# Kernel optimization log

Hardware: AMD Instinct MI355X
Metric: run time of the kernel (lower is better)

The kernel has to match this reference:

```python
import jax, jax.numpy as jnp
import numpy as np

ALPHA = 0.2  # LeakyReLU negative slope
EPS = 1e-6


def gam(x):
    # relu6(x+3)/3 + eps
    return jnp.clip(x + 3.0, 0.0, 6.0) / 3.0 + EPS


def leaky(x):
    return jnp.where(x >= 0, x, ALPHA * x)


def relu_bt(x):
    # threshold at detached inf-norm of input: min(leaky_relu(x), ||x||_inf)
    t = jax.lax.stop_gradient(jnp.max(jnp.abs(x)))
    return jnp.minimum(leaky(x), t)


def setup_inputs() -> dict:
    key = jax.random.key(0)
    ks = jax.random.split(key, 8)
    N, E, Din, Dout = 100000, 1600000, 256, 64
    return {
        "input": jax.random.normal(ks[0], (N, Din), dtype=jnp.float32),
        "edge": jax.random.randint(ks[1], (2, E), 0, N, dtype=jnp.int32),
        "W_high": jax.random.normal(ks[2], (Din, Dout), dtype=jnp.float32) * 0.06,
        "W_low": jax.random.normal(ks[3], (Din, Dout), dtype=jnp.float32) * 0.06,
        "a_high": jax.random.normal(ks[4], (1, 4 * Dout), dtype=jnp.float32) * 0.09,
        "a_low": jax.random.normal(ks[5], (1, 4 * Dout), dtype=jnp.float32) * 0.09,
        "c_high": jax.random.uniform(ks[6], (1, 1), dtype=jnp.float32),
        "c_low": jax.random.uniform(ks[7], (1, 1), dtype=jnp.float32),
    }


def reference(input, edge, W_high, W_low, a_high, a_low, c_high, c_low):
    N = input.shape[0]
    F = W_high.shape[1]
    src, dst = edge[0], edge[1]

    theta_high = gam(c_high) / 2.0  # [1,1]
    theta_low = gam(c_low) / 2.0

    h_high = relu_bt(input @ W_high)  # [N,F]
    h_low = relu_bt(input @ W_low)

    hh_s, hh_d = h_high[src], h_high[dst]  # [E,F]
    hl_s, hl_d = h_low[src], h_low[dst]

    ah = a_high[0]
    al = a_low[0]
    # a . [h_i, h_j, h_i+h_j, h_i-h_j] folded into per-endpoint coefficients
    # NOTE: original code uses h_high for the first two blocks of the LOW branch too.
    score_high = hh_s @ (ah[:F] + ah[2 * F:3 * F] + ah[3 * F:]) \
               + hh_d @ (ah[F:2 * F] + ah[2 * F:3 * F] - ah[3 * F:])  # [E]
    score_low = hh_s @ al[:F] + hh_d @ al[F:2 * F] \
              + hl_s @ (al[2 * F:3 * F] + al[3 * F:]) \
              + hl_d @ (al[2 * F:3 * F] - al[3 * F:])

    e_high = jnp.exp(-leaky(score_high / jnp.linalg.norm(a_high)))  # [E]
    e_low = jnp.exp(-leaky(score_low / jnp.linalg.norm(a_low)))

    # sparse COO spmm: rowsum and weighted aggregation
    rowsum_high = jax.ops.segment_sum(e_high, src, num_segments=N)[:, None]  # [N,1]
    rowsum_low = jax.ops.segment_sum(e_low, src, num_segments=N)[:, None]
    hp_high = jax.ops.segment_sum(e_high[:, None] * hh_d, src, num_segments=N)  # [N,F]
    hp_low = jax.ops.segment_sum(e_low[:, None] * hl_d, src, num_segments=N)

    hp_high = hp_high / (rowsum_high + theta_high)
    hp_low = hp_low / (rowsum_low + theta_low)

    # concat=True branch
    return relu_bt(jnp.concatenate([hp_high, hp_low], axis=1))  # [N,2F]
```

## Files before the change

kernel.cpp:

```cpp
#include <hip/hip_runtime.h>
#include <hip/hip_bf16.h>
#include <hip/hip_fp16.h>
#include <math.h>

typedef unsigned short ushort_t;
typedef unsigned int uint_t;
typedef __attribute__((ext_vector_type(8))) short short8;
typedef __attribute__((ext_vector_type(4))) float floatx4;
typedef __attribute__((ext_vector_type(4))) uint_t uintx4;

#define ALPHA 0.2f
#define CAP 64
#define NXCD 8

__device__ __forceinline__ float leaky(float x) { return x >= 0.0f ? x : ALPHA * x; }

__device__ __forceinline__ float bf2f(ushort_t u) {
    union { uint_t i; float f; } v; v.i = ((uint_t)u) << 16; return v.f;
}
__device__ __forceinline__ float bflo(uint_t p) {
    union { uint_t i; float f; } v; v.i = p << 16; return v.f;
}
__device__ __forceinline__ float bfhi(uint_t p) {
    union { uint_t i; float f; } v; v.i = p & 0xffff0000u; return v.f;
}
__device__ __forceinline__ ushort_t f2bf(float f) {
    union { float f; uint_t i; } v; v.f = f;
    return (ushort_t)((v.i + 0x8000u) >> 16);
}
__device__ __forceinline__ uint_t pack_bf2(float a, float b) {
    union { float f; uint_t i; } ua, ub; ua.f = a; ub.f = b;
    return ((ua.i + 0x8000u) >> 16) | ((ub.i + 0x8000u) & 0xffff0000u);
}

__global__ void prep_wtrans_kernel(const float* __restrict__ Wh, const float* __restrict__ Wl,
                                   ushort_t* __restrict__ WTg,
                                   const float* __restrict__ ah, const float* __restrict__ al,
                                   const float* __restrict__ ch, const float* __restrict__ cl,
                                   float* __restrict__ coef, float* __restrict__ consts) {
    int t = threadIdx.x;
    if (blockIdx.x < 128) {
        int c = blockIdx.x;
        float v = (c < 64) ? Wh[t * 64 + c] : Wl[t * 64 + (c - 64)];
        WTg[c * 256 + t] = f2bf(v);
        return;
    }
    __shared__ float red[256];
    float va = ah[t];
    red[t] = va * va;
    __syncthreads();
    for (int s = 128; s > 0; s >>= 1) { if (t < s) red[t] += red[t + s]; __syncthreads(); }
    float sum_h = red[0];
    __syncthreads();
    float vb = al[t];
    red[t] = vb * vb;
    __syncthreads();
    for (int s = 128; s > 0; s >>= 1) { if (t < s) red[t] += red[t + s]; __syncthreads(); }
    float sum_l = red[0];

    if (t == 0) {
        consts[0] = 1.0f / sqrtf(sum_h);
        consts[1] = 1.0f / sqrtf(sum_l);
        float c = ch[0];
        float g = fminf(fmaxf(c + 3.0f, 0.0f), 6.0f) / 3.0f + 1e-6f;
        consts[2] = g * 0.5f;
        c = cl[0];
        g = fminf(fmaxf(c + 3.0f, 0.0f), 6.0f) / 3.0f + 1e-6f;
        consts[3] = g * 0.5f;
    }
    if (t < 128) {
        int f = t;
        float c0, c1, c2, c3;
        if (f < 64) {
            c0 = ah[f] + ah[128 + f] + ah[192 + f];
            c1 = ah[64 + f] + ah[128 + f] - ah[192 + f];
            c2 = al[f];
            c3 = al[64 + f];
        } else {
            int g = f - 64;
            c0 = 0.0f;
            c1 = 0.0f;
            c2 = al[128 + g] + al[192 + g];
            c3 = al[128 + g] - al[192 + g];
        }
        coef[0 * 128 + f] = c0;
        coef[1 * 128 + f] = c1;
        coef[2 * 128 + f] = c2;
        coef[3 * 128 + f] = c3;
    }
}

__global__ __launch_bounds__(256, 4) void gemm_kernel(const float* __restrict__ in,
                                                      const ushort_t* __restrict__ WTg,
                                                      const float* __restrict__ coef,
                                                      ushort_t* __restrict__ hcat,
                                                      float* __restrict__ s4, int N) {
    __shared__ ushort_t WT[128 * 128];
    __shared__ float coefS[512];
    int tid = threadIdx.x;
    for (int i = tid; i < 512; i += 256) coefS[i] = coef[i];

    int wave = tid >> 6, lane = tid & 63;
    int quad = lane >> 4, m16 = lane & 15;
    int rowbase = blockIdx.x * 64 + wave * 16;
    int arow = rowbase + m16;
    if (arow >= N) arow = N - 1;

    floatx4 acc[8];
#pragma unroll
    for (int ct = 0; ct < 8; ++ct) acc[ct] = (floatx4){0.0f, 0.0f, 0.0f, 0.0f};

    const uint4* WTg4 = (const uint4*)WTg;

#pragma unroll
    for (int kh = 0; kh < 2; ++kh) {
        if (kh) __syncthreads();
        for (int i = tid; i < 2048; i += 256) {
            int c = i >> 4, j = i & 15;
            int sj = j ^ (c & 7);
            uint4 v = WTg4[c * 32 + kh * 16 + j];
            *(uint4*)&WT[c * 128 + sj * 8] = v;
        }
        __syncthreads();
#pragma unroll
        for (int ks = 0; ks < 4; ++ks) {
            const float* ap = in + (size_t)arow * 256 + kh * 128 + ks * 32 + quad * 8;
            float4 a0 = *(const float4*)ap;
            float4 a1 = *(const float4*)(ap + 4);
            union { uintx4 u; short8 s; } av;
            av.u[0] = pack_bf2(a0.x, a0.y);
            av.u[1] = pack_bf2(a0.z, a0.w);
            av.u[2] = pack_bf2(a1.x, a1.y);
            av.u[3] = pack_bf2(a1.z, a1.w);
#pragma unroll
            for (int ct = 0; ct < 8; ++ct) {
                int c = ct * 16 + m16;
                int sch = (ks * 4 + quad) ^ (c & 7);
                short8 b = *(const short8*)&WT[c * 128 + sch * 8];
                acc[ct] = __builtin_amdgcn_mfma_f32_16x16x32_bf16(av.s, b, acc[ct], 0, 0, 0);
            }
        }
    }

    float hv[8][4];
#pragma unroll
    for (int ct = 0; ct < 8; ++ct) {
#pragma unroll
        for (int r = 0; r < 4; ++r) {
            int row = rowbase + quad * 4 + r;
            float v = leaky(acc[ct][r]);
            hv[ct][r] = v;
            if (row < N) hcat[(size_t)row * 128 + ct * 16 + m16] = f2bf(v);
        }
    }
#pragma unroll
    for (int r = 0; r < 4; ++r) {
        int row = rowbase + quad * 4 + r;
        float p0 = 0, p1 = 0, p2 = 0, p3 = 0;
#pragma unroll
        for (int ct = 0; ct < 8; ++ct) {
            int c = ct * 16 + m16;
            float h = hv[ct][r];
            p0 += coefS[c] * h;
            p1 += coefS[128 + c] * h;
            p2 += coefS[256 + c] * h;
            p3 += coefS[384 + c] * h;
        }
#pragma unroll
        for (int off = 1; off < 16; off <<= 1) {
            p0 += __shfl_xor(p0, off);
            p1 += __shfl_xor(p1, off);
            p2 += __shfl_xor(p2, off);
            p3 += __shfl_xor(p3, off);
        }
        if (m16 == 0 && row < N) {
            floatx4 v = {p0, p1, p2, p3};
            *(floatx4*)&s4[(size_t)row * 4] = v;
        }
    }
}

__global__ __launch_bounds__(256) void scatter_kernel(const int* __restrict__ edge,
                                                      int* __restrict__ cursor,
                                                      uint_t* __restrict__ elist,
                                                      int E, int N) {
    int xcd = blockIdx.x & (NXCD - 1);
    int chunk = blockIdx.x >> 3;
    int nchunks = gridDim.x >> 3;
    int TN = (N + NXCD - 1) / NXCD;
    int lo = xcd * TN;
    int hiN = lo + TN;
    int stride = nchunks * 256;
    for (int e = chunk * 256 + threadIdx.x; e < E; e += stride) {
        int src = edge[e];
        if (src >= lo && src < hiN) {
            int dst = edge[E + e];
            int pos = atomicAdd(&cursor[src], 1);
            if (pos < CAP) elist[(size_t)src * CAP + pos] = (uint_t)dst;
        }
    }
}

__global__ __launch_bounds__(256) void aggregate_kernel(const int* __restrict__ deg,
                                                        const uint_t* __restrict__ elist,
                                                        const ushort_t* __restrict__ hcat,
                                                        const float* __restrict__ s4,
                                                        const float* __restrict__ consts,
                                                        float* __restrict__ out, int N) {
    int w = (blockIdx.x * blockDim.x + threadIdx.x) >> 6;
    int lane = threadIdx.x & 63;
    if (w >= N) return;
    int d = deg[w];
    if (d > CAP) d = CAP;

    float s_own_h = s4[(size_t)w * 4 + 0];
    float s_own_l = s4[(size_t)w * 4 + 2];
    float inv_h = consts[0], inv_l = consts[1];
    int dst = 0;
    float wh = 0.0f, wl = 0.0f;
    if (lane < d) {
        dst = (int)elist[(size_t)w * CAP + lane];
        float4 sv = *(const float4*)&s4[(size_t)dst * 4];
        wh = __expf(-leaky((s_own_h + sv.y) * inv_h));
        wl = __expf(-leaky((s_own_l + sv.w) * inv_l));
    }
    uint_t wp = (uint_t)__half_as_ushort(__float2half(wh))
              | ((uint_t)__half_as_ushort(__float2half(wl)) << 16);
    float rsh = wh, rsl = wl;
#pragma unroll
    for (int off = 1; off < 64; off <<= 1) {
        rsh += __shfl_xor(rsh, off);
        rsl += __shfl_xor(rsl, off);
    }

    bool hi = lane < 32;
    int wsh = hi ? 0 : 16;
    const ushort_t* hbase = hcat + lane * 2;

    float a0 = 0, a1 = 0, b0 = 0, b1 = 0;
    int j = 0;
    for (; j + 4 <= d; j += 4) {
        int d0 = __shfl(dst, j);
        int d1 = __shfl(dst, j + 1);
        int d2 = __shfl(dst, j + 2);
        int d3 = __shfl(dst, j + 3);
        uint_t u0 = (uint_t)__shfl((int)wp, j);
        uint_t u1 = (uint_t)__shfl((int)wp, j + 1);
        uint_t u2 = (uint_t)__shfl((int)wp, j + 2);
        uint_t u3 = (uint_t)__shfl((int)wp, j + 3);
        uint_t p0 = *(const uint_t*)&hbase[(size_t)d0 * 128];
        uint_t p1 = *(const uint_t*)&hbase[(size_t)d1 * 128];
        uint_t p2 = *(const uint_t*)&hbase[(size_t)d2 * 128];
        uint_t p3 = *(const uint_t*)&hbase[(size_t)d3 * 128];
        float w0 = __half2float(__ushort_as_half((ushort_t)(u0 >> wsh)));
        float w1 = __half2float(__ushort_as_half((ushort_t)(u1 >> wsh)));
        float w2 = __half2float(__ushort_as_half((ushort_t)(u2 >> wsh)));
        float w3 = __half2float(__ushort_as_half((ushort_t)(u3 >> wsh)));
        a0 += w0 * bflo(p0); a1 += w0 * bfhi(p0);
        b0 += w1 * bflo(p1); b1 += w1 * bfhi(p1);
        a0 += w2 * bflo(p2); a1 += w2 * bfhi(p2);
        b0 += w3 * bflo(p3); b1 += w3 * bfhi(p3);
    }
    for (; j < d; ++j) {
        int dj = __shfl(dst, j);
        uint_t uj = (uint_t)__shfl((int)wp, j);
        uint_t p = *(const uint_t*)&hbase[(size_t)dj * 128];
        float wt = __half2float(__ushort_as_half((ushort_t)(uj >> wsh)));
        a0 += wt * bflo(p);
        a1 += wt * bfhi(p);
    }

    float acc0 = a0 + b0;
    float acc1 = a1 + b1;
    float rsum = hi ? rsh : rsl;
    float theta = hi ? consts[2] : consts[3];
    float inv = 1.0f / (rsum + theta);
    float2 r;
    r.x = leaky(acc0 * inv);
    r.y = leaky(acc1 * inv);
    *(float2*)&out[(size_t)w * 128 + lane * 2] = r;
}

extern "C" void kernel_launch(void* const* d_in, const int* in_sizes, int n_in,
                              void* d_out, int out_size, void* d_ws, size_t ws_size,
                              hipStream_t stream) {
    const float* input = (const float*)d_in[0];
    const int* edge = (const int*)d_in[1];
    const float* Wh = (const float*)d_in[2];
    const float* Wl = (const float*)d_in[3];
    const float* ah = (const float*)d_in[4];
    const float* al = (const float*)d_in[5];
    const float* ch = (const float*)d_in[6];
    const float* cl = (const float*)d_in[7];
    int N = in_sizes[0] / 256;
    int E = in_sizes[1] / 2;
    float* out = (float*)d_out;

    char* ws = (char*)d_ws;
    size_t off = 0;
    uint_t* elist = (uint_t*)(ws + off);     off += (size_t)N * CAP * 4;
    ushort_t* hcat = (ushort_t*)(ws + off);  off += (size_t)N * 128 * 2;
    float* s4 = (float*)(ws + off);          off += (size_t)N * 4 * 4;
    int* cursor = (int*)(ws + off);          off += (size_t)N * 4;
    ushort_t* WTg = (ushort_t*)(ws + off);   off += 128 * 256 * 2;
    float* coef = (float*)(ws + off);        off += 4 * 128 * 4;
    float* consts = (float*)(ws + off);      off += 64;

    hipMemsetAsync(cursor, 0, (size_t)N * 4, stream);
    prep_wtrans_kernel<<<129, 256, 0, stream>>>(Wh, Wl, WTg, ah, al, ch, cl, coef, consts);
    gemm_kernel<<<(N + 63) / 64, 256, 0, stream>>>(input, WTg, coef, hcat, s4, N);
    int nchunks = (E + 256 * 8 - 1) / (256 * 8);
    scatter_kernel<<<nchunks * NXCD, 256, 0, stream>>>(edge, cursor, elist, E, N);
    aggregate_kernel<<<(N + 3) / 4, 256, 0, stream>>>(cursor, elist, hcat, s4, consts, out, N);
}
```

Measured before the change: 356.5 us.

## Merge edge scatter into GEMM launch so both run concurrently

Fuses the edge-bucketing scatter and the projection GEMM into one launch. The first Gscat blocks do the scatter and the remaining blocks do the GEMM, so the latency-bound atomic scatter overlaps with the compute-bound GEMM and one kernel launch boundary goes away. The scatter now reads four source indices per thread with nontemporal vector loads and uses a fixed chunk count. The GEMM input loads also become nontemporal. The combined kernel carries the GEMM's shared memory footprint into the scatter blocks, which can lower their occupancy.

```diff
diff --git a/kernel.cpp b/kernel.cpp
--- a/kernel.cpp
+++ b/kernel.cpp
@@ -8,6 +8,7 @@
 typedef __attribute__((ext_vector_type(8))) short short8;
 typedef __attribute__((ext_vector_type(4))) float floatx4;
 typedef __attribute__((ext_vector_type(4))) uint_t uintx4;
+typedef __attribute__((ext_vector_type(4))) int intx4;
 
 #define ALPHA 0.2f
 #define CAP 64
@@ -90,19 +91,51 @@
     }
 }
 
-__global__ __launch_bounds__(256, 4) void gemm_kernel(const float* __restrict__ in,
-                                                      const ushort_t* __restrict__ WTg,
-                                                      const float* __restrict__ coef,
-                                                      ushort_t* __restrict__ hcat,
-                                                      float* __restrict__ s4, int N) {
+__global__ __launch_bounds__(256, 4) void gemm_scatter_kernel(
+        const float* __restrict__ in, const ushort_t* __restrict__ WTg,
+        const float* __restrict__ coef, ushort_t* __restrict__ hcat,
+        float* __restrict__ s4, const int* __restrict__ edge,
+        int* __restrict__ cursor, uint_t* __restrict__ elist,
+        int N, int E, int Gscat) {
     __shared__ ushort_t WT[128 * 128];
     __shared__ float coefS[512];
+
+    if ((int)blockIdx.x < Gscat) {
+        int xcd = blockIdx.x & (NXCD - 1);
+        int chunk = blockIdx.x >> 3;
+        int nchunks = Gscat >> 3;
+        int TN = (N + NXCD - 1) / NXCD;
+        int lo = xcd * TN;
+        int hiN = lo + TN;
+        int base = (chunk * 256 + threadIdx.x) * 4;
+        int stride = nchunks * 256 * 4;
+        for (int e = base; e < E; e += stride) {
+            intx4 sv;
+            if (e + 4 <= E) {
+                sv = __builtin_nontemporal_load((const intx4*)(edge + e));
+            } else {
+#pragma unroll
+                for (int j = 0; j < 4; ++j) sv[j] = (e + j < E) ? edge[e + j] : -1;
+            }
+#pragma unroll
+            for (int j = 0; j < 4; ++j) {
+                int src = sv[j];
+                if (src >= lo && src < hiN) {
+                    int dst = __builtin_nontemporal_load(edge + E + e + j);
+                    int pos = atomicAdd(&cursor[src], 1);
+                    if (pos < CAP) elist[(size_t)src * CAP + pos] = (uint_t)dst;
+                }
+            }
+        }
+        return;
+    }
+
     int tid = threadIdx.x;
     for (int i = tid; i < 512; i += 256) coefS[i] = coef[i];
 
     int wave = tid >> 6, lane = tid & 63;
     int quad = lane >> 4, m16 = lane & 15;
-    int rowbase = blockIdx.x * 64 + wave * 16;
+    int rowbase = (blockIdx.x - Gscat) * 64 + wave * 16;
     int arow = rowbase + m16;
     if (arow >= N) arow = N - 1;
 
@@ -124,14 +157,14 @@
         __syncthreads();
 #pragma unroll
         for (int ks = 0; ks < 4; ++ks) {
-            const float* ap = in + (size_t)arow * 256 + kh * 128 + ks * 32 + quad * 8;
-            float4 a0 = *(const float4*)ap;
-            float4 a1 = *(const float4*)(ap + 4);
+            const floatx4* ap = (const floatx4*)(in + (size_t)arow * 256 + kh * 128 + ks * 32 + quad * 8);
+            floatx4 a0 = __builtin_nontemporal_load(ap);
+            floatx4 a1 = __builtin_nontemporal_load(ap + 1);
             union { uintx4 u; short8 s; } av;
-            av.u[0] = pack_bf2(a0.x, a0.y);
-            av.u[1] = pack_bf2(a0.z, a0.w);
-            av.u[2] = pack_bf2(a1.x, a1.y);
-            av.u[3] = pack_bf2(a1.z, a1.w);
+            av.u[0] = pack_bf2(a0[0], a0[1]);
+            av.u[1] = pack_bf2(a0[2], a0[3]);
+            av.u[2] = pack_bf2(a1[0], a1[1]);
+            av.u[3] = pack_bf2(a1[2], a1[3]);
 #pragma unroll
             for (int ct = 0; ct < 8; ++ct) {
                 int c = ct * 16 + m16;
@@ -176,27 +209,6 @@
         if (m16 == 0 && row < N) {
             floatx4 v = {p0, p1, p2, p3};
             *(floatx4*)&s4[(size_t)row * 4] = v;
-        }
-    }
-}
-
-__global__ __launch_bounds__(256) void scatter_kernel(const int* __restrict__ edge,
-                                                      int* __restrict__ cursor,
-                                                      uint_t* __restrict__ elist,
-                                                      int E, int N) {
-    int xcd = blockIdx.x & (NXCD - 1);
-    int chunk = blockIdx.x >> 3;
-    int nchunks = gridDim.x >> 3;
-    int TN = (N + NXCD - 1) / NXCD;
-    int lo = xcd * TN;
-    int hiN = lo + TN;
-    int stride = nchunks * 256;
-    for (int e = chunk * 256 + threadIdx.x; e < E; e += stride) {
-        int src = edge[e];
-        if (src >= lo && src < hiN) {
-            int dst = edge[E + e];
-            int pos = atomicAdd(&cursor[src], 1);
-            if (pos < CAP) elist[(size_t)src * CAP + pos] = (uint_t)dst;
         }
     }
 }
@@ -308,8 +320,10 @@
 
     hipMemsetAsync(cursor, 0, (size_t)N * 4, stream);
     prep_wtrans_kernel<<<129, 256, 0, stream>>>(Wh, Wl, WTg, ah, al, ch, cl, coef, consts);
-    gemm_kernel<<<(N + 63) / 64, 256, 0, stream>>>(input, WTg, coef, hcat, s4, N);
-    int nchunks = (E + 256 * 8 - 1) / (256 * 8);
-    scatter_kernel<<<nchunks * NXCD, 256, 0, stream>>>(edge, cursor, elist, E, N);
+    int Ggemm = (N + 63) / 64;
+    int nchunks = 256;
+    int Gscat = nchunks * NXCD;
+    gemm_scatter_kernel<<<Gscat + Ggemm, 256, 0, stream>>>(input, WTg, coef, hcat, s4,
+                                                           edge, cursor, elist, N, E, Gscat);
     aggregate_kernel<<<(N + 3) / 4, 256, 0, stream>>>(cursor, elist, hcat, s4, consts, out, N);
 }
```

Result: no change. 362.2 us (+1.6%).
